# Performance work log

Measured on AMD Instinct MI355X. Metric: run time of the kernel, lower is better.

The kernel has to match this reference:

```python
import jax, jax.numpy as jnp
import numpy as np

# torch.rrelu in eval mode uses slope = (lower+upper)/2 = (1/8 + 1/3)/2
RRELU_SLOPE = (1.0 / 8.0 + 1.0 / 3.0) / 2.0

N_NODES = 50000
N_EDGES = 800000
EMB_FEATS = 128
IN_FEATS = 128
HIDDEN = 64


def setup_inputs() -> dict:
    key = jax.random.key(0)
    ks = jax.random.split(key, 16)
    z = jax.random.normal(ks[0], (N_NODES, EMB_FEATS), dtype=jnp.float32)
    x = jax.random.normal(ks[1], (N_NODES, IN_FEATS), dtype=jnp.float32)
    edge_index = jax.random.randint(ks[2], (2, N_EDGES), 0, N_NODES, dtype=jnp.int32)

    def glorot(k, shape):
        fan_in, fan_out = shape
        lim = jnp.sqrt(6.0 / (fan_in + fan_out))
        return jax.random.uniform(k, shape, jnp.float32, -lim, lim)

    return {
        "z": z,
        "x": x,
        "edge_index": edge_index,
        "W_e1": glorot(ks[3], (EMB_FEATS, HIDDEN)),
        "b_e1": jnp.zeros((HIDDEN,), jnp.float32),
        "W_e2": glorot(ks[4], (HIDDEN, HIDDEN)),
        "b_e2": jnp.zeros((HIDDEN,), jnp.float32),
        "W_f1": glorot(ks[5], (IN_FEATS, HIDDEN)),
        "b_f1": jnp.zeros((HIDDEN,), jnp.float32),
        "W_f2": glorot(ks[6], (HIDDEN, HIDDEN)),
        "b_f2": jnp.zeros((HIDDEN,), jnp.float32),
        "W_out": glorot(ks[7], (HIDDEN, 1)),
        "b_out": jnp.zeros((1,), jnp.float32),
    }


def gcn_conv(h_in, W, b, src, dst, n_nodes):
    """PyG GCNConv: self-loops + symmetric deg^-1/2 normalization."""
    h = h_in @ W  # [N, out]
    # degree of self-loop-augmented graph: indeg + 1
    indeg = jax.ops.segment_sum(
        jnp.ones(dst.shape[0], h.dtype), dst, num_segments=n_nodes)
    deg = indeg + 1.0
    dinv = jnp.where(deg > 0, 1.0 / jnp.sqrt(deg), 0.0)  # [N]
    norm = dinv[src] * dinv[dst]  # [E]
    # neighbor messages (gather + scatter-add)
    agg = jax.ops.segment_sum(h[src] * norm[:, None], dst, num_segments=n_nodes)
    # self-loop contribution: dinv[i]*dinv[i]*h[i]
    agg = agg + h * (dinv * dinv)[:, None]
    return agg + b


def _rrelu(t):
    return jnp.where(t >= 0, t, t * RRELU_SLOPE)


def reference(z, x, edge_index, W_e1, b_e1, W_e2, b_e2,
              W_f1, b_f1, W_f2, b_f2, W_out, b_out):
    src, dst = edge_index[0], edge_index[1]
    n = z.shape[0]
    ze = _rrelu(gcn_conv(z, W_e1, b_e1, src, dst, n))
    ze = jnp.tanh(gcn_conv(ze, W_e2, b_e2, src, dst, n))
    xf = _rrelu(gcn_conv(x, W_f1, b_f1, src, dst, n))
    xf = jnp.tanh(gcn_conv(xf, W_f2, b_f2, src, dst, n))
    return (ze * xf) @ W_out + b_out  # [N, 1]
```

## Files before the change

### kernel.cpp

```cpp
#include <hip/hip_runtime.h>
#include <hip/hip_fp16.h>
#include <math.h>

#define RRELU_SLOPE 0.22916667f


__global__ __launch_bounds__(256) void k_zero(int* __restrict__ cnt, int N) {
    int i = blockIdx.x * 256 + threadIdx.x;
    if (i < N) cnt[i] = 0;
}

__global__ __launch_bounds__(256) void k_deg(const int* __restrict__ dst, int E,
                                             int* __restrict__ cnt,
                                             int* __restrict__ rank) {
    int e = blockIdx.x * 256 + threadIdx.x;
    if (e < E) rank[e] = atomicAdd(&cnt[dst[e]], 1);
}

__global__ __launch_bounds__(256) void k_scan1(const int* __restrict__ cnt, int N,
                                               int* __restrict__ bsum) {
    int i = blockIdx.x * 256 + threadIdx.x;
    int v = (i < N) ? cnt[i] : 0;
    for (int o = 32; o >= 1; o >>= 1) v += __shfl_xor(v, o, 64);
    __shared__ int ws[4];
    if ((threadIdx.x & 63) == 0) ws[threadIdx.x >> 6] = v;
    __syncthreads();
    if (threadIdx.x == 0) bsum[blockIdx.x] = ws[0] + ws[1] + ws[2] + ws[3];
}

__global__ __launch_bounds__(256) void k_scan2(const int* __restrict__ bsum, int NB,
                                               int* __restrict__ boff,
                                               int* __restrict__ rowp, int N, int E) {
    __shared__ int s[256];
    int t = threadIdx.x;
    int v[4];
    int loc = 0;
    for (int i = 0; i < 4; i++) {
        int idx = t * 4 + i;
        v[i] = (idx < NB) ? bsum[idx] : 0;
        loc += v[i];
    }
    s[t] = loc;
    __syncthreads();
    for (int o = 1; o < 256; o <<= 1) {
        int u = (t >= o) ? s[t - o] : 0;
        __syncthreads();
        s[t] += u;
        __syncthreads();
    }
    int excl = s[t] - loc;
    for (int i = 0; i < 4; i++) {
        int idx = t * 4 + i;
        if (idx < NB) { boff[idx] = excl; excl += v[i]; }
    }
    if (t == 0) rowp[N] = E;
}

__global__ __launch_bounds__(256) void k_scan3(const int* __restrict__ cnt,
                                               const int* __restrict__ boff, int N,
                                               int* __restrict__ rowp,
                                               float* __restrict__ dinv) {
    int i = blockIdx.x * 256 + threadIdx.x;
    int lane = threadIdx.x & 63, wid = threadIdx.x >> 6;
    int v = (i < N) ? cnt[i] : 0;
    int inc = v;
    for (int o = 1; o < 64; o <<= 1) {
        int u = __shfl_up(inc, o, 64);
        if (lane >= o) inc += u;
    }
    __shared__ int wsum[4];
    if (lane == 63) wsum[wid] = inc;
    __syncthreads();
    int wo = 0;
    for (int w = 0; w < wid; w++) wo += wsum[w];
    if (i < N) {
        int excl = inc - v + wo + boff[blockIdx.x];
        rowp[i] = excl;
        dinv[i] = 1.0f / sqrtf((float)v + 1.0f);
    }
}

__global__ __launch_bounds__(256) void k_fill(const int* __restrict__ src,
                                              const int* __restrict__ dst,
                                              const int* __restrict__ rank, int E,
                                              const int* __restrict__ rowp,
                                              int* __restrict__ csrc) {
    int e = blockIdx.x * 256 + threadIdx.x;
    if (e >= E) return;
    int d = dst[e];
    csrc[rowp[d] + rank[e]] = src[e];
}

__global__ __launch_bounds__(256) void k_mm1(const float* __restrict__ A0,
                                             const float* __restrict__ A1,
                                             const float* __restrict__ W0,
                                             const float* __restrict__ W1,
                                             const float* __restrict__ dinv,
                                             __half* __restrict__ Hh, int N) {
    const float* A = blockIdx.y ? A1 : A0;
    const float* W = blockIdx.y ? W1 : W0;
    __half* H = Hh + blockIdx.y * 64;

    __shared__ float As[64][20];
    __shared__ float Ws[16][64];

    const int tid = threadIdx.x;
    const int tc = tid & 15, tr = tid >> 4;
    const int row0 = blockIdx.x * 64;
    const int srow = tid >> 2, sk = (tid & 3) * 4;
    const int wk = tid >> 4, wc = (tid & 15) * 4;

    float acc[4][4] = {};

    for (int k0 = 0; k0 < 128; k0 += 16) {
        float4 av = make_float4(0.f, 0.f, 0.f, 0.f);
        int gr = row0 + srow;
        if (gr < N) av = *(const float4*)(A + (size_t)gr * 128 + k0 + sk);
        float4 wv = *(const float4*)(W + (size_t)(k0 + wk) * 64 + wc);
        __syncthreads();
        *(float4*)&As[srow][sk] = av;
        *(float4*)&Ws[wk][wc] = wv;
        __syncthreads();

#pragma unroll
        for (int k = 0; k < 16; k += 4) {
            float4 a4[4], w4[4];
#pragma unroll
            for (int i = 0; i < 4; i++) a4[i] = *(const float4*)&As[tr * 4 + i][k];
#pragma unroll
            for (int kk = 0; kk < 4; kk++) w4[kk] = *(const float4*)&Ws[k + kk][tc * 4];
#pragma unroll
            for (int i = 0; i < 4; i++) {
                const float* ap = (const float*)&a4[i];
#pragma unroll
                for (int kk = 0; kk < 4; kk++) {
                    const float* wp = (const float*)&w4[kk];
                    float a = ap[kk];
                    acc[i][0] = fmaf(a, wp[0], acc[i][0]);
                    acc[i][1] = fmaf(a, wp[1], acc[i][1]);
                    acc[i][2] = fmaf(a, wp[2], acc[i][2]);
                    acc[i][3] = fmaf(a, wp[3], acc[i][3]);
                }
            }
        }
    }

#pragma unroll
    for (int i = 0; i < 4; i++) {
        int r = row0 + tr * 4 + i;
        if (r < N) {
            float dv = dinv[r];
            union { __half2 h2[2]; uint2 u; } pk;
            pk.h2[0] = __floats2half2_rn(acc[i][0] * dv, acc[i][1] * dv);
            pk.h2[1] = __floats2half2_rn(acc[i][2] * dv, acc[i][3] * dv);
            *(uint2*)(H + (size_t)r * 128 + tc * 4) = pk.u;
        }
    }
}

__global__ __launch_bounds__(256) void k_mm2h(const __half* __restrict__ A0,
                                              const __half* __restrict__ A1,
                                              const float* __restrict__ W0,
                                              const float* __restrict__ W1,
                                              const float* __restrict__ dinv,
                                              __half* __restrict__ Hh, int N) {
    const __half* A = blockIdx.y ? A1 : A0;
    const float* W = blockIdx.y ? W1 : W0;
    __half* H = Hh + blockIdx.y * 64;

    __shared__ float As[64][20];
    __shared__ float Ws[16][64];

    const int tid = threadIdx.x;
    const int tc = tid & 15, tr = tid >> 4;
    const int row0 = blockIdx.x * 64;
    const int srow = tid >> 2, sk = (tid & 3) * 4;
    const int wk = tid >> 4, wc = (tid & 15) * 4;

    float acc[4][4] = {};

    for (int k0 = 0; k0 < 64; k0 += 16) {
        float4 av = make_float4(0.f, 0.f, 0.f, 0.f);
        int gr = row0 + srow;
        if (gr < N) {
            union { uint2 u; __half2 h2[2]; } cu;
            cu.u = *(const uint2*)(A + (size_t)gr * 64 + k0 + sk);
            float2 f01 = __half22float2(cu.h2[0]);
            float2 f23 = __half22float2(cu.h2[1]);
            av = make_float4(f01.x, f01.y, f23.x, f23.y);
        }
        float4 wv = *(const float4*)(W + (size_t)(k0 + wk) * 64 + wc);
        __syncthreads();
        *(float4*)&As[srow][sk] = av;
        *(float4*)&Ws[wk][wc] = wv;
        __syncthreads();

#pragma unroll
        for (int k = 0; k < 16; k += 4) {
            float4 a4[4], w4[4];
#pragma unroll
            for (int i = 0; i < 4; i++) a4[i] = *(const float4*)&As[tr * 4 + i][k];
#pragma unroll
            for (int kk = 0; kk < 4; kk++) w4[kk] = *(const float4*)&Ws[k + kk][tc * 4];
#pragma unroll
            for (int i = 0; i < 4; i++) {
                const float* ap = (const float*)&a4[i];
#pragma unroll
                for (int kk = 0; kk < 4; kk++) {
                    const float* wp = (const float*)&w4[kk];
                    float a = ap[kk];
                    acc[i][0] = fmaf(a, wp[0], acc[i][0]);
                    acc[i][1] = fmaf(a, wp[1], acc[i][1]);
                    acc[i][2] = fmaf(a, wp[2], acc[i][2]);
                    acc[i][3] = fmaf(a, wp[3], acc[i][3]);
                }
            }
        }
    }

#pragma unroll
    for (int i = 0; i < 4; i++) {
        int r = row0 + tr * 4 + i;
        if (r < N) {
            float dv = dinv[r];
            union { __half2 h2[2]; uint2 u; } pk;
            pk.h2[0] = __floats2half2_rn(acc[i][0] * dv, acc[i][1] * dv);
            pk.h2[1] = __floats2half2_rn(acc[i][2] * dv, acc[i][3] * dv);
            *(uint2*)(H + (size_t)r * 128 + tc * 4) = pk.u;
        }
    }
}

#define GATHER_ADD8(S, C)                                      \
    {                                                          \
        union { uint4 u; __half2 h2[4]; } g_;                  \
        g_.u = *(const uint4*)(Hp + (size_t)(C) * 128);        \
        float2 f0_ = __half22float2(g_.h2[0]);                 \
        float2 f1_ = __half22float2(g_.h2[1]);                 \
        float2 f2_ = __half22float2(g_.h2[2]);                 \
        float2 f3_ = __half22float2(g_.h2[3]);                 \
        S[0] += f0_.x; S[1] += f0_.y; S[2] += f1_.x;           \
        S[3] += f1_.y; S[4] += f2_.x; S[5] += f2_.y;           \
        S[6] += f3_.x; S[7] += f3_.y;                          \
    }

#define AGG_LOOP()                                                          \
    int beg = rowp[i], end = rowp[i + 1];                                   \
    float s0[8] = {}, s1[8] = {}, s2[8] = {}, s3[8] = {};                   \
    int p = beg;                                                            \
    for (; p + 16 <= end; p += 16) {                                        \
        int cA = csrc[p + e];                                               \
        int cB = csrc[p + 4 + e];                                           \
        int cC = csrc[p + 8 + e];                                           \
        int cD = csrc[p + 12 + e];                                          \
        GATHER_ADD8(s0, cA);                                                \
        GATHER_ADD8(s1, cB);                                                \
        GATHER_ADD8(s2, cC);                                                \
        GATHER_ADD8(s3, cD);                                                \
    }                                                                       \
    for (; p + 8 <= end; p += 8) {                                          \
        int cA = csrc[p + e];                                               \
        int cB = csrc[p + 4 + e];                                           \
        GATHER_ADD8(s0, cA);                                                \
        GATHER_ADD8(s1, cB);                                                \
    }                                                                       \
    if (p + 4 <= end) {                                                     \
        int cA = csrc[p + e];                                               \
        GATHER_ADD8(s0, cA);                                                \
        p += 4;                                                             \
    }                                                                       \
    {                                                                       \
        int rem = end - p;                                                  \
        if (rem > 0) {                                                      \
            int c = csrc[p + ((e < rem) ? e : 0)];                          \
            if (e < rem) GATHER_ADD8(s1, c);                                \
        }                                                                   \
    }                                                                       \
    float s[8];                                                             \
    _Pragma("unroll")                                                       \
    for (int k = 0; k < 8; k++)                                             \
        s[k] = (s0[k] + s1[k]) + (s2[k] + s3[k]);                           \
    _Pragma("unroll")                                                       \
    for (int k = 0; k < 8; k++) s[k] += __shfl_xor(s[k], 16, 64);           \
    _Pragma("unroll")                                                       \
    for (int k = 0; k < 8; k++) s[k] += __shfl_xor(s[k], 32, 64);

__global__ __launch_bounds__(256) void k_agg_act(
    const int* __restrict__ rowp, const int* __restrict__ csrc,
    const float* __restrict__ dinv, const __half* __restrict__ Hh, int N,
    const float* __restrict__ bz, const float* __restrict__ bx,
    __half* __restrict__ azh, __half* __restrict__ axh) {
    int wid = threadIdx.x >> 6, lane = threadIdx.x & 63;
    int i = blockIdx.x * 4 + wid;
    if (i >= N) return;
    int g = lane & 7;
    int h = (lane >> 3) & 1;
    int e = lane >> 4;
    const __half* Hp = Hh + h * 64 + g * 8;
    AGG_LOOP();

    if (e == 0) {
        float sl[8] = {};
        GATHER_ADD8(sl, i);
        float dvi = dinv[i];
        const float* bb = h ? bx : bz;
        float4 b0 = *(const float4*)(bb + g * 8);
        float4 b1 = *(const float4*)(bb + g * 8 + 4);
        float r[8];
        const float* bp = (const float*)&b0;
#pragma unroll
        for (int k = 0; k < 4; k++) r[k] = fmaf(dvi, s[k] + sl[k], bp[k]);
        bp = (const float*)&b1;
#pragma unroll
        for (int k = 0; k < 4; k++) r[4 + k] = fmaf(dvi, s[4 + k] + sl[4 + k], bp[k]);
#pragma unroll
        for (int k = 0; k < 8; k++) r[k] = r[k] >= 0.f ? r[k] : r[k] * RRELU_SLOPE;
        __half* ap = h ? axh : azh;
        union { __half2 h2[4]; uint4 u; } pk;
        pk.h2[0] = __floats2half2_rn(r[0], r[1]);
        pk.h2[1] = __floats2half2_rn(r[2], r[3]);
        pk.h2[2] = __floats2half2_rn(r[4], r[5]);
        pk.h2[3] = __floats2half2_rn(r[6], r[7]);
        *(uint4*)(ap + (size_t)i * 64 + g * 8) = pk.u;
    }
}

__global__ __launch_bounds__(256) void k_agg_final(
    const int* __restrict__ rowp, const int* __restrict__ csrc,
    const float* __restrict__ dinv, const __half* __restrict__ Hh, int N,
    const float* __restrict__ bz, const float* __restrict__ bx,
    const float* __restrict__ Wout, const float* __restrict__ bout,
    float* __restrict__ out) {
    int wid = threadIdx.x >> 6, lane = threadIdx.x & 63;
    int i = blockIdx.x * 4 + wid;
    if (i >= N) return;
    int g = lane & 7;
    int h = (lane >> 3) & 1;
    int e = lane >> 4;
    const __half* Hp = Hh + h * 64 + g * 8;
    AGG_LOOP();

    float sl[8] = {};
    GATHER_ADD8(sl, i);
    float dvi = dinv[i];
    const float* bb = h ? bx : bz;
    float4 b0 = *(const float4*)(bb + g * 8);
    float4 b1 = *(const float4*)(bb + g * 8 + 4);
    float t[8];
    const float* bp = (const float*)&b0;
#pragma unroll
    for (int k = 0; k < 4; k++) t[k] = tanhf(fmaf(dvi, s[k] + sl[k], bp[k]));
    bp = (const float*)&b1;
#pragma unroll
    for (int k = 0; k < 4; k++)
        t[4 + k] = tanhf(fmaf(dvi, s[4 + k] + sl[4 + k], bp[k]));
    float4 w0 = *(const float4*)(Wout + g * 8);
    float4 w1 = *(const float4*)(Wout + g * 8 + 4);
    float prod = 0.f;
    const float* wp = (const float*)&w0;
#pragma unroll
    for (int k = 0; k < 4; k++) prod = fmaf(t[k] * __shfl_xor(t[k], 8, 64), wp[k], prod);
    wp = (const float*)&w1;
#pragma unroll
    for (int k = 0; k < 4; k++)
        prod = fmaf(t[4 + k] * __shfl_xor(t[4 + k], 8, 64), wp[k], prod);
    for (int o = 4; o >= 1; o >>= 1) prod += __shfl_xor(prod, o, 64);
    if (lane == 0) out[i] = prod + bout[0];
}


extern "C" void kernel_launch(void* const* d_in, const int* in_sizes, int n_in,
                              void* d_out, int out_size, void* d_ws, size_t ws_size,
                              hipStream_t stream) {
    const float* z = (const float*)d_in[0];
    const float* x = (const float*)d_in[1];
    const int* ei = (const int*)d_in[2];
    const float* We1 = (const float*)d_in[3];
    const float* be1 = (const float*)d_in[4];
    const float* We2 = (const float*)d_in[5];
    const float* be2 = (const float*)d_in[6];
    const float* Wf1 = (const float*)d_in[7];
    const float* bf1 = (const float*)d_in[8];
    const float* Wf2 = (const float*)d_in[9];
    const float* bf2 = (const float*)d_in[10];
    const float* Wout = (const float*)d_in[11];
    const float* bout = (const float*)d_in[12];
    float* out = (float*)d_out;

    int N = in_sizes[0] / 128;
    int E = in_sizes[2] / 2;
    const int* src = ei;
    const int* dst = ei + E;

    char* base = (char*)d_ws;
    size_t off = 0;
    auto take = [&](size_t nbytes) -> char* {
        char* p = base + off;
        off = (off + nbytes + 255) & ~(size_t)255;
        return p;
    };
    int NB = (N + 255) / 256;
    int* cnt = (int*)take((size_t)N * 4);
    int* bsum = (int*)take(1024 * 4);
    int* boff = (int*)take(1024 * 4);
    int* rowp = (int*)take(((size_t)N + 1) * 4);
    float* dinv = (float*)take((size_t)N * 4);
    int* rank = (int*)take((size_t)E * 4);
    int* csrc = (int*)take((size_t)E * 4);
    __half* Hh = (__half*)take((size_t)N * 128 * 2);
    __half* azh = (__half*)take((size_t)N * 64 * 2);
    __half* axh = (__half*)take((size_t)N * 64 * 2);

    int egrid = (E + 255) / 256;
    k_zero<<<NB, 256, 0, stream>>>(cnt, N);
    k_deg<<<egrid, 256, 0, stream>>>(dst, E, cnt, rank);
    k_scan1<<<NB, 256, 0, stream>>>(cnt, N, bsum);
    k_scan2<<<1, 256, 0, stream>>>(bsum, NB, boff, rowp, N, E);
    k_scan3<<<NB, 256, 0, stream>>>(cnt, boff, N, rowp, dinv);
    k_fill<<<egrid, 256, 0, stream>>>(src, dst, rank, E, rowp, csrc);

    dim3 mmgrid((N + 63) / 64, 2);
    int agrid = (N + 3) / 4;

    k_mm1<<<mmgrid, 256, 0, stream>>>(z, x, We1, Wf1, dinv, Hh, N);
    k_agg_act<<<agrid, 256, 0, stream>>>(rowp, csrc, dinv, Hh, N, be1, bf1, azh, axh);
    k_mm2h<<<mmgrid, 256, 0, stream>>>(azh, axh, We2, Wf2, dinv, Hh, N);
    k_agg_final<<<agrid, 256, 0, stream>>>(rowp, csrc, dinv, Hh, N, be2, bf2, Wout,
                                           bout, out);
}
```

Before: 187.4 us.

## Fuse CSR construction into one cooperative kernel with grid-wide syncs

Replaces six small kernels (zero, degree count, three scan passes, fill) with a single cooperative kernel of 512 blocks that uses grid.sync between phases. The single-block middle scan is replaced by each block summing the prior block totals itself. This removes several launch gaps and per-kernel drain/fill overhead. In exchange it adds grid barrier costs, fewer threads for the edge passes, and redundant partial-sum reads of bsum.

```diff
diff --git a/kernel.cpp b/kernel.cpp
--- a/kernel.cpp
+++ b/kernel.cpp
@@ -1,94 +1,81 @@
 #include <hip/hip_runtime.h>
 #include <hip/hip_fp16.h>
+#include <hip/hip_cooperative_groups.h>
 #include <math.h>
 
+namespace cg = cooperative_groups;
+
 #define RRELU_SLOPE 0.22916667f
 
-
-__global__ __launch_bounds__(256) void k_zero(int* __restrict__ cnt, int N) {
-    int i = blockIdx.x * 256 + threadIdx.x;
-    if (i < N) cnt[i] = 0;
-}
-
-__global__ __launch_bounds__(256) void k_deg(const int* __restrict__ dst, int E,
-                                             int* __restrict__ cnt,
-                                             int* __restrict__ rank) {
-    int e = blockIdx.x * 256 + threadIdx.x;
-    if (e < E) rank[e] = atomicAdd(&cnt[dst[e]], 1);
-}
-
-__global__ __launch_bounds__(256) void k_scan1(const int* __restrict__ cnt, int N,
-                                               int* __restrict__ bsum) {
-    int i = blockIdx.x * 256 + threadIdx.x;
-    int v = (i < N) ? cnt[i] : 0;
-    for (int o = 32; o >= 1; o >>= 1) v += __shfl_xor(v, o, 64);
-    __shared__ int ws[4];
-    if ((threadIdx.x & 63) == 0) ws[threadIdx.x >> 6] = v;
-    __syncthreads();
-    if (threadIdx.x == 0) bsum[blockIdx.x] = ws[0] + ws[1] + ws[2] + ws[3];
-}
-
-__global__ __launch_bounds__(256) void k_scan2(const int* __restrict__ bsum, int NB,
-                                               int* __restrict__ boff,
-                                               int* __restrict__ rowp, int N, int E) {
-    __shared__ int s[256];
-    int t = threadIdx.x;
-    int v[4];
-    int loc = 0;
-    for (int i = 0; i < 4; i++) {
-        int idx = t * 4 + i;
-        v[i] = (idx < NB) ? bsum[idx] : 0;
-        loc += v[i];
-    }
-    s[t] = loc;
-    __syncthreads();
-    for (int o = 1; o < 256; o <<= 1) {
-        int u = (t >= o) ? s[t - o] : 0;
-        __syncthreads();
-        s[t] += u;
-        __syncthreads();
-    }
-    int excl = s[t] - loc;
-    for (int i = 0; i < 4; i++) {
-        int idx = t * 4 + i;
-        if (idx < NB) { boff[idx] = excl; excl += v[i]; }
-    }
-    if (t == 0) rowp[N] = E;
-}
-
-__global__ __launch_bounds__(256) void k_scan3(const int* __restrict__ cnt,
-                                               const int* __restrict__ boff, int N,
-                                               int* __restrict__ rowp,
-                                               float* __restrict__ dinv) {
-    int i = blockIdx.x * 256 + threadIdx.x;
-    int lane = threadIdx.x & 63, wid = threadIdx.x >> 6;
-    int v = (i < N) ? cnt[i] : 0;
-    int inc = v;
-    for (int o = 1; o < 64; o <<= 1) {
-        int u = __shfl_up(inc, o, 64);
-        if (lane >= o) inc += u;
-    }
-    __shared__ int wsum[4];
-    if (lane == 63) wsum[wid] = inc;
-    __syncthreads();
-    int wo = 0;
-    for (int w = 0; w < wid; w++) wo += wsum[w];
-    if (i < N) {
-        int excl = inc - v + wo + boff[blockIdx.x];
-        rowp[i] = excl;
-        dinv[i] = 1.0f / sqrtf((float)v + 1.0f);
-    }
-}
-
-__global__ __launch_bounds__(256) void k_fill(const int* __restrict__ src,
-                                              const int* __restrict__ dst,
-                                              const int* __restrict__ rank, int E,
-                                              const int* __restrict__ rowp,
-                                              int* __restrict__ csrc) {
-    int e = blockIdx.x * 256 + threadIdx.x;
-    if (e >= E) return;
-    int d = dst[e];
-    csrc[rowp[d] + rank[e]] = src[e];
+__global__ __launch_bounds__(256) void k_csr(const int* __restrict__ src,
+                                             const int* __restrict__ dst, int E,
+                                             int N, int* __restrict__ cnt,
+                                             int* __restrict__ rank,
+                                             int* __restrict__ bsum,
+                                             int* __restrict__ rowp,
+                                             float* __restrict__ dinv,
+                                             int* __restrict__ csrc) {
+    cg::grid_group grid = cg::this_grid();
+    const int tid = blockIdx.x * 256 + threadIdx.x;
+    const int nthr = gridDim.x * 256;
+    const int NB = (N + 255) / 256;
+
+    for (int i = tid; i < N; i += nthr) cnt[i] = 0;
+    grid.sync();
+
+    for (int e = tid; e < E; e += nthr) rank[e] = atomicAdd(&cnt[dst[e]], 1);
+    grid.sync();
+
+    {
+        __shared__ int ws[4];
+        for (int c = blockIdx.x; c < NB; c += gridDim.x) {
+            int i = c * 256 + threadIdx.x;
+            int v = (i < N) ? cnt[i] : 0;
+            for (int o = 32; o >= 1; o >>= 1) v += __shfl_xor(v, o, 64);
+            if ((threadIdx.x & 63) == 0) ws[threadIdx.x >> 6] = v;
+            __syncthreads();
+            if (threadIdx.x == 0) bsum[c] = ws[0] + ws[1] + ws[2] + ws[3];
+            __syncthreads();
+        }
+    }
+    grid.sync();
+
+    {
+        __shared__ int s_boff;
+        __shared__ int wsum[4];
+        for (int c = blockIdx.x; c < NB; c += gridDim.x) {
+            if (threadIdx.x < 64) {
+                int acc = 0;
+                for (int j = threadIdx.x; j < c; j += 64) acc += bsum[j];
+                for (int o = 32; o >= 1; o >>= 1) acc += __shfl_xor(acc, o, 64);
+                if (threadIdx.x == 0) s_boff = acc;
+            }
+            int i = c * 256 + threadIdx.x;
+            int lane = threadIdx.x & 63, wid = threadIdx.x >> 6;
+            int v = (i < N) ? cnt[i] : 0;
+            int inc = v;
+            for (int o = 1; o < 64; o <<= 1) {
+                int u = __shfl_up(inc, o, 64);
+                if (lane >= o) inc += u;
+            }
+            if (lane == 63) wsum[wid] = inc;
+            __syncthreads();
+            int wo = 0;
+            for (int w = 0; w < wid; w++) wo += wsum[w];
+            if (i < N) {
+                rowp[i] = inc - v + wo + s_boff;
+                dinv[i] = 1.0f / sqrtf((float)v + 1.0f);
+            }
+            __syncthreads();
+        }
+        if (tid == 0) rowp[N] = E;
+    }
+    grid.sync();
+
+    for (int e = tid; e < E; e += nthr) {
+        int d = dst[e];
+        csrc[rowp[d] + rank[e]] = src[e];
+    }
 }
 
 __global__ __launch_bounds__(256) void k_mm1(const float* __restrict__ A0,
@@ -399,10 +386,8 @@
         off = (off + nbytes + 255) & ~(size_t)255;
         return p;
     };
-    int NB = (N + 255) / 256;
     int* cnt = (int*)take((size_t)N * 4);
     int* bsum = (int*)take(1024 * 4);
-    int* boff = (int*)take(1024 * 4);
     int* rowp = (int*)take(((size_t)N + 1) * 4);
     float* dinv = (float*)take((size_t)N * 4);
     int* rank = (int*)take((size_t)E * 4);
@@ -411,13 +396,11 @@
     __half* azh = (__half*)take((size_t)N * 64 * 2);
     __half* axh = (__half*)take((size_t)N * 64 * 2);
 
-    int egrid = (E + 255) / 256;
-    k_zero<<<NB, 256, 0, stream>>>(cnt, N);
-    k_deg<<<egrid, 256, 0, stream>>>(dst, E, cnt, rank);
-    k_scan1<<<NB, 256, 0, stream>>>(cnt, N, bsum);
-    k_scan2<<<1, 256, 0, stream>>>(bsum, NB, boff, rowp, N, E);
-    k_scan3<<<NB, 256, 0, stream>>>(cnt, boff, N, rowp, dinv);
-    k_fill<<<egrid, 256, 0, stream>>>(src, dst, rank, E, rowp, csrc);
+    void* kargs[] = {(void*)&src, (void*)&dst, (void*)&E, (void*)&N,
+                     (void*)&cnt, (void*)&rank, (void*)&bsum, (void*)&rowp,
+                     (void*)&dinv, (void*)&csrc};
+    hipLaunchCooperativeKernel((const void*)k_csr, dim3(512), dim3(256), kargs, 0,
+                               stream);
 
     dim3 mmgrid((N + 63) / 64, 2);
     int agrid = (N + 3) / 4;
```

Result: slower. 384.1 us (+104.9%).
